# Kernel tuning notes

Measured on AMD Instinct MI355X. Metric: run time of the kernel, lower is better.

The kernel has to match this reference:

```python
import jax, jax.numpy as jnp
import numpy as np

B, C = 65536, 1000  # batch, num_classes


def setup_inputs() -> dict:
    key = jax.random.key(0)
    k1, k2, k3 = jax.random.split(key, 3)
    # Sub-models end in Softmax, so outputs are probability distributions.
    output1 = jax.nn.softmax(jax.random.normal(k1, (B, C), dtype=jnp.float32), axis=-1)
    output2 = jax.nn.softmax(jax.random.normal(k2, (B, C), dtype=jnp.float32), axis=-1)
    output3 = jax.nn.softmax(jax.random.normal(k3, (B, C), dtype=jnp.float32), axis=-1)
    return {"output1": output1, "output2": output2, "output3": output3}


def reference(output1, output2, output3):
    # Per-sample argmax predictions of each ensemble member: [B]
    pred1 = jnp.argmax(output1, axis=-1)
    pred2 = jnp.argmax(output2, axis=-1)
    pred3 = jnp.argmax(output3, axis=-1)

    # Vectorized equivalent of bincount(3 votes, minlength=C) -> argmax -> count:
    # with 3 voters, the histogram max is 3 (all agree), 2 (a pair agrees), or 1 (tie).
    eq12 = pred1 == pred2
    eq13 = pred1 == pred3
    eq23 = pred2 == pred3
    count_max = jnp.where(eq12 & eq13, 3, jnp.where(eq12 | eq13 | eq23, 2, 1))  # [B] int
    maj = jnp.where(eq12 | eq13, pred1, jnp.where(eq23, pred2, pred1))
    # Tie (count_max < 2) falls back to model 3's prediction, as in the tf.cond.
    value = jnp.where(count_max < 2, pred3, maj)  # [B]

    # Average probability vector over the members whose prediction == chosen class.
    m1 = (pred1 == value).astype(output1.dtype)[:, None]
    m2 = (pred2 == value).astype(output2.dtype)[:, None]
    m3 = (pred3 == value).astype(output3.dtype)[:, None]
    denom = count_max.astype(output1.dtype)[:, None]
    avg_correct_prob = (output1 * m1 + output2 * m2 + output3 * m3) / denom  # [B, C]

    avg_prob = (output1 + output2 + output3) / jnp.asarray(3.0, output1.dtype)  # [B, C]

    pred_output = value.astype(jnp.int64)
    return pred_output, avg_correct_prob, avg_prob
```

## Files before the change

### kernel.cpp

```cpp
#include <hip/hip_runtime.h>


#define NUM_C   1000
#define NUM_C4  250

__device__ __forceinline__ unsigned long long pk(float v, int idx) {
    return ((unsigned long long)__float_as_uint(v) << 32) | (unsigned int)(~idx);
}
__device__ __forceinline__ unsigned long long pmax(unsigned long long a,
                                                   unsigned long long b) {
    return a > b ? a : b;
}

__global__ __launch_bounds__(256) void ensemble3_kernel(
    const float* __restrict__ o1, const float* __restrict__ o2,
    const float* __restrict__ o3,
    float* __restrict__ acp,
    float* __restrict__ avg,
    float* __restrict__ pred_f,
    long long* __restrict__ pred_i)
{
    const int row = blockIdx.x;
    const int tid = threadIdx.x;
    const long long base = (long long)row * NUM_C;

    float4 v1 = make_float4(0.f, 0.f, 0.f, 0.f);
    float4 v2 = v1, v3 = v1;
    unsigned long long p1 = 0ull, p2 = 0ull, p3 = 0ull;
    const bool active = tid < NUM_C4;

    if (active) {
        const long long off = base + 4LL * tid;
        v1 = *(const float4*)(o1 + off);
        v2 = *(const float4*)(o2 + off);
        v3 = *(const float4*)(o3 + off);
        const int i0 = 4 * tid;
        p1 = pmax(pmax(pk(v1.x, i0),     pk(v1.y, i0 + 1)),
                  pmax(pk(v1.z, i0 + 2), pk(v1.w, i0 + 3)));
        p2 = pmax(pmax(pk(v2.x, i0),     pk(v2.y, i0 + 1)),
                  pmax(pk(v2.z, i0 + 2), pk(v2.w, i0 + 3)));
        p3 = pmax(pmax(pk(v3.x, i0),     pk(v3.y, i0 + 1)),
                  pmax(pk(v3.z, i0 + 2), pk(v3.w, i0 + 3)));
    }

    #pragma unroll
    for (int off = 32; off > 0; off >>= 1) {
        p1 = pmax(p1, __shfl_xor(p1, off));
        p2 = pmax(p2, __shfl_xor(p2, off));
        p3 = pmax(p3, __shfl_xor(p3, off));
    }
    __shared__ unsigned long long red[3][4];
    const int wave = tid >> 6;
    if ((tid & 63) == 0) {
        red[0][wave] = p1; red[1][wave] = p2; red[2][wave] = p3;
    }
    __syncthreads();
    const unsigned long long q1 =
        pmax(pmax(red[0][0], red[0][1]), pmax(red[0][2], red[0][3]));
    const unsigned long long q2 =
        pmax(pmax(red[1][0], red[1][1]), pmax(red[1][2], red[1][3]));
    const unsigned long long q3 =
        pmax(pmax(red[2][0], red[2][1]), pmax(red[2][2], red[2][3]));
    const int pred1 = (int)(~(unsigned int)q1);
    const int pred2 = (int)(~(unsigned int)q2);
    const int pred3 = (int)(~(unsigned int)q3);

    const bool eq12 = pred1 == pred2;
    const bool eq13 = pred1 == pred3;
    const bool eq23 = pred2 == pred3;
    const int cmax  = (eq12 && eq13) ? 3 : ((eq12 || eq13 || eq23) ? 2 : 1);
    const int maj   = (eq12 || eq13) ? pred1 : (eq23 ? pred2 : pred1);
    const int value = (cmax < 2) ? pred3 : maj;

    if (tid == 0) {
        if (pred_i) pred_i[row] = (long long)value;
        else        pred_f[row] = (float)value;
    }

    if (active) {
        const float m1 = (pred1 == value) ? 1.0f : 0.0f;
        const float m2 = (pred2 == value) ? 1.0f : 0.0f;
        const float m3 = (pred3 == value) ? 1.0f : 0.0f;
        const float denom = (float)cmax;

        float4 a, g;
        a.x = (v1.x * m1 + v2.x * m2 + v3.x * m3) / denom;
        a.y = (v1.y * m1 + v2.y * m2 + v3.y * m3) / denom;
        a.z = (v1.z * m1 + v2.z * m2 + v3.z * m3) / denom;
        a.w = (v1.w * m1 + v2.w * m2 + v3.w * m3) / denom;
        g.x = (v1.x + v2.x + v3.x) / 3.0f;
        g.y = (v1.y + v2.y + v3.y) / 3.0f;
        g.z = (v1.z + v2.z + v3.z) / 3.0f;
        g.w = (v1.w + v2.w + v3.w) / 3.0f;

        const long long off = base + 4LL * tid;
        *(float4*)(acp + off) = a;
        *(float4*)(avg + off) = g;
    }
}

extern "C" void kernel_launch(void* const* d_in, const int* in_sizes, int n_in,
                              void* d_out, int out_size, void* d_ws, size_t ws_size,
                              hipStream_t stream) {
    const float* o1 = (const float*)d_in[0];
    const float* o2 = (const float*)d_in[1];
    const float* o3 = (const float*)d_in[2];

    const long long BC = in_sizes[0];
    const long long B  = BC / NUM_C;

    float* outf = (float*)d_out;
    float*     pred_f = nullptr;
    long long* pred_i = nullptr;
    float*     acp;
    float*     avg;

    if ((long long)out_size == 2LL * B + 2LL * BC) {
        pred_i = (long long*)d_out;
        acp = outf + 2LL * B;
    } else {
        pred_f = outf;
        acp = outf + B;
    }
    avg = acp + BC;

    ensemble3_kernel<<<dim3((unsigned)B), dim3(256), 0, stream>>>(
        o1, o2, o3, acp, avg, pred_f, pred_i);
}
```

Baseline: 972.7 us.

## Map one row per wave and drop block-level shared-memory reduction

Each 64-lane wave now handles a full row, with every lane loading up to four float4 chunks from each of the three inputs. Four rows share a 256-thread block. The argmax reduction uses only wave shuffles, removing the shared-memory write and __syncthreads. This is meant to raise loads in flight per thread and cut synchronization overhead, at the cost of more registers per thread.

```diff
diff --git a/kernel.cpp b/kernel.cpp
--- a/kernel.cpp
+++ b/kernel.cpp
@@ -1,8 +1,9 @@
 #include <hip/hip_runtime.h>
 
 
-#define NUM_C   1000
-#define NUM_C4  250
+#define NUM_C 1000
+#define C4    250
+#define RPB   4
 
 __device__ __forceinline__ unsigned long long pk(float v, int idx) {
     return ((unsigned long long)__float_as_uint(v) << 32) | (unsigned int)(~idx);
@@ -18,52 +19,52 @@
     float* __restrict__ acp,
     float* __restrict__ avg,
     float* __restrict__ pred_f,
-    long long* __restrict__ pred_i)
+    long long* __restrict__ pred_i,
+    int nrows)
 {
-    const int row = blockIdx.x;
-    const int tid = threadIdx.x;
+    const int wave = threadIdx.x >> 6;
+    const int lane = threadIdx.x & 63;
+    const int row  = blockIdx.x * RPB + wave;
+    if (row >= nrows) return;
     const long long base = (long long)row * NUM_C;
 
-    float4 v1 = make_float4(0.f, 0.f, 0.f, 0.f);
-    float4 v2 = v1, v3 = v1;
-    unsigned long long p1 = 0ull, p2 = 0ull, p3 = 0ull;
-    const bool active = tid < NUM_C4;
+    const float4 z4 = make_float4(0.f, 0.f, 0.f, 0.f);
+    float4 v1[4], v2[4], v3[4];
 
-    if (active) {
-        const long long off = base + 4LL * tid;
-        v1 = *(const float4*)(o1 + off);
-        v2 = *(const float4*)(o2 + off);
-        v3 = *(const float4*)(o3 + off);
-        const int i0 = 4 * tid;
-        p1 = pmax(pmax(pk(v1.x, i0),     pk(v1.y, i0 + 1)),
-                  pmax(pk(v1.z, i0 + 2), pk(v1.w, i0 + 3)));
-        p2 = pmax(pmax(pk(v2.x, i0),     pk(v2.y, i0 + 1)),
-                  pmax(pk(v2.z, i0 + 2), pk(v2.w, i0 + 3)));
-        p3 = pmax(pmax(pk(v3.x, i0),     pk(v3.y, i0 + 1)),
-                  pmax(pk(v3.z, i0 + 2), pk(v3.w, i0 + 3)));
+    #pragma unroll
+    for (int j = 0; j < 4; ++j) {
+        const int c4 = j * 64 + lane;
+        if (c4 < C4) {
+            const long long off = base + 4LL * c4;
+            v1[j] = *(const float4*)(o1 + off);
+            v2[j] = *(const float4*)(o2 + off);
+            v3[j] = *(const float4*)(o3 + off);
+        } else {
+            v1[j] = z4; v2[j] = z4; v3[j] = z4;
+        }
+    }
+
+    unsigned long long k1 = 0ull, k2 = 0ull, k3 = 0ull;
+    #pragma unroll
+    for (int j = 0; j < 4; ++j) {
+        const int i0 = (j * 64 + lane) * 4;
+        k1 = pmax(k1, pmax(pmax(pk(v1[j].x, i0),     pk(v1[j].y, i0 + 1)),
+                           pmax(pk(v1[j].z, i0 + 2), pk(v1[j].w, i0 + 3))));
+        k2 = pmax(k2, pmax(pmax(pk(v2[j].x, i0),     pk(v2[j].y, i0 + 1)),
+                           pmax(pk(v2[j].z, i0 + 2), pk(v2[j].w, i0 + 3))));
+        k3 = pmax(k3, pmax(pmax(pk(v3[j].x, i0),     pk(v3[j].y, i0 + 1)),
+                           pmax(pk(v3[j].z, i0 + 2), pk(v3[j].w, i0 + 3))));
     }
 
     #pragma unroll
     for (int off = 32; off > 0; off >>= 1) {
-        p1 = pmax(p1, __shfl_xor(p1, off));
-        p2 = pmax(p2, __shfl_xor(p2, off));
-        p3 = pmax(p3, __shfl_xor(p3, off));
+        k1 = pmax(k1, __shfl_xor(k1, off));
+        k2 = pmax(k2, __shfl_xor(k2, off));
+        k3 = pmax(k3, __shfl_xor(k3, off));
     }
-    __shared__ unsigned long long red[3][4];
-    const int wave = tid >> 6;
-    if ((tid & 63) == 0) {
-        red[0][wave] = p1; red[1][wave] = p2; red[2][wave] = p3;
-    }
-    __syncthreads();
-    const unsigned long long q1 =
-        pmax(pmax(red[0][0], red[0][1]), pmax(red[0][2], red[0][3]));
-    const unsigned long long q2 =
-        pmax(pmax(red[1][0], red[1][1]), pmax(red[1][2], red[1][3]));
-    const unsigned long long q3 =
-        pmax(pmax(red[2][0], red[2][1]), pmax(red[2][2], red[2][3]));
-    const int pred1 = (int)(~(unsigned int)q1);
-    const int pred2 = (int)(~(unsigned int)q2);
-    const int pred3 = (int)(~(unsigned int)q3);
+    const int pred1 = (int)(~(unsigned int)k1);
+    const int pred2 = (int)(~(unsigned int)k2);
+    const int pred3 = (int)(~(unsigned int)k3);
 
     const bool eq12 = pred1 == pred2;
     const bool eq13 = pred1 == pred3;
@@ -72,30 +73,33 @@
     const int maj   = (eq12 || eq13) ? pred1 : (eq23 ? pred2 : pred1);
     const int value = (cmax < 2) ? pred3 : maj;
 
-    if (tid == 0) {
+    if (lane == 0) {
         if (pred_i) pred_i[row] = (long long)value;
         else        pred_f[row] = (float)value;
     }
 
-    if (active) {
-        const float m1 = (pred1 == value) ? 1.0f : 0.0f;
-        const float m2 = (pred2 == value) ? 1.0f : 0.0f;
-        const float m3 = (pred3 == value) ? 1.0f : 0.0f;
-        const float denom = (float)cmax;
+    const float m1 = (pred1 == value) ? 1.0f : 0.0f;
+    const float m2 = (pred2 == value) ? 1.0f : 0.0f;
+    const float m3 = (pred3 == value) ? 1.0f : 0.0f;
+    const float denom = (float)cmax;
 
-        float4 a, g;
-        a.x = (v1.x * m1 + v2.x * m2 + v3.x * m3) / denom;
-        a.y = (v1.y * m1 + v2.y * m2 + v3.y * m3) / denom;
-        a.z = (v1.z * m1 + v2.z * m2 + v3.z * m3) / denom;
-        a.w = (v1.w * m1 + v2.w * m2 + v3.w * m3) / denom;
-        g.x = (v1.x + v2.x + v3.x) / 3.0f;
-        g.y = (v1.y + v2.y + v3.y) / 3.0f;
-        g.z = (v1.z + v2.z + v3.z) / 3.0f;
-        g.w = (v1.w + v2.w + v3.w) / 3.0f;
-
-        const long long off = base + 4LL * tid;
-        *(float4*)(acp + off) = a;
-        *(float4*)(avg + off) = g;
+    #pragma unroll
+    for (int j = 0; j < 4; ++j) {
+        const int c4 = j * 64 + lane;
+        if (c4 < C4) {
+            float4 a, g;
+            a.x = (v1[j].x * m1 + v2[j].x * m2 + v3[j].x * m3) / denom;
+            a.y = (v1[j].y * m1 + v2[j].y * m2 + v3[j].y * m3) / denom;
+            a.z = (v1[j].z * m1 + v2[j].z * m2 + v3[j].z * m3) / denom;
+            a.w = (v1[j].w * m1 + v2[j].w * m2 + v3[j].w * m3) / denom;
+            g.x = (v1[j].x + v2[j].x + v3[j].x) / 3.0f;
+            g.y = (v1[j].y + v2[j].y + v3[j].y) / 3.0f;
+            g.z = (v1[j].z + v2[j].z + v3[j].z) / 3.0f;
+            g.w = (v1[j].w + v2[j].w + v3[j].w) / 3.0f;
+            const long long off = base + 4LL * c4;
+            *(float4*)(acp + off) = a;
+            *(float4*)(avg + off) = g;
+        }
     }
 }
 
@@ -113,7 +117,6 @@
     float*     pred_f = nullptr;
     long long* pred_i = nullptr;
     float*     acp;
-    float*     avg;
 
     if ((long long)out_size == 2LL * B + 2LL * BC) {
         pred_i = (long long*)d_out;
@@ -122,8 +125,9 @@
         pred_f = outf;
         acp = outf + B;
     }
-    avg = acp + BC;
+    float* avg = acp + BC;
 
-    ensemble3_kernel<<<dim3((unsigned)B), dim3(256), 0, stream>>>(
-        o1, o2, o3, acp, avg, pred_f, pred_i);
+    const int nblocks = (int)((B + RPB - 1) / RPB);
+    ensemble3_kernel<<<dim3(nblocks), dim3(256), 0, stream>>>(
+        o1, o2, o3, acp, avg, pred_f, pred_i, (int)B);
 }
```

Result: no change. 974.7 us (+0.2%).
